# Performance work log

Hardware: AMD Instinct MI355X
Metric: run time of the kernel (lower is better)

Reference implementation:

```python
import jax, jax.numpy as jnp
import numpy as np

B, S, D, H = 4, 2048, 1024, 16
HD = D // H

def setup_inputs() -> dict:
    key = jax.random.key(0)
    ks = jax.random.split(key, 11)
    s = 1.0 / np.sqrt(D)
    return {
        "q": jax.random.normal(ks[0], (B, S, D), jnp.float32),
        "k": jax.random.normal(ks[1], (B, S, D), jnp.float32),
        "v": jax.random.normal(ks[2], (B, S, D), jnp.float32),
        "Wq": jax.random.normal(ks[3], (D, D), jnp.float32) * s,
        "bq": jax.random.normal(ks[4], (D,), jnp.float32) * 0.01,
        "Wk": jax.random.normal(ks[5], (D, D), jnp.float32) * s,
        "bk": jax.random.normal(ks[6], (D,), jnp.float32) * 0.01,
        "Wv": jax.random.normal(ks[7], (D, D), jnp.float32) * s,
        "bv": jax.random.normal(ks[8], (D,), jnp.float32) * 0.01,
        "Wo": jax.random.normal(ks[9], (D, D), jnp.float32) * s,
        "bo": jax.random.normal(ks[10], (D,), jnp.float32) * 0.01,
    }

def reference(q, k, v, Wq, bq, Wk, bk, Wv, bv, Wo, bo):
    # linear projections + ReLU activation (as in the torch module)
    qh = jax.nn.relu(q @ Wq.T + bq)
    kh = jax.nn.relu(k @ Wk.T + bk)
    vh = jax.nn.relu(v @ Wv.T + bv)
    # split heads: [B,S,D] -> [B,H,S,HD]
    def split(x):
        return x.reshape(B, S, H, HD).transpose(0, 2, 1, 3)
    qh, kh, vh = split(qh), split(kh), split(vh)
    scale = 1.0 / np.sqrt(HD).astype(np.float32)
    scores = jnp.einsum("bhqd,bhkd->bhqk", qh, kh) * scale
    attn = jax.nn.softmax(scores, axis=-1)
    y = jnp.einsum("bhqk,bhkd->bhqd", attn, vh)
    # merge heads: [B,H,S,HD] -> [B,S,D]
    y = y.transpose(0, 2, 1, 3).reshape(B, S, D)
    return jax.nn.relu(y @ Wo.T + bo)
```

## Files before the change

### kernel.cpp

```cpp
#include <hip/hip_runtime.h>
#include <hip/hip_bf16.h>
#include <cstdint>
#include <cstddef>

#define Bc 4
#define Sc 2048
#define Dc 1024
#define Hc 16

typedef __bf16 bf16;
typedef bf16  bf16x4 __attribute__((ext_vector_type(4)));
typedef bf16  bf16x8 __attribute__((ext_vector_type(8)));
typedef float f32x4  __attribute__((ext_vector_type(4)));

__device__ __forceinline__ void load_lds16(const bf16* g, bf16* l) {
    __builtin_amdgcn_global_load_lds((const __attribute__((address_space(1))) void*)g,
                                     (__attribute__((address_space(3))) void*)l,
                                     16, 0, 0);
}

__device__ __forceinline__ void cvt16(const float* __restrict__ g,
                                      bf16x8& lo, bf16x8& hi) {
    const f32x4 a0 = *(const f32x4*)(g);
    const f32x4 a1 = *(const f32x4*)(g + 4);
    const f32x4 a2 = *(const f32x4*)(g + 8);
    const f32x4 a3 = *(const f32x4*)(g + 12);
#pragma unroll
    for (int j = 0; j < 4; j++) {
        lo[j]     = (bf16)a0[j];
        lo[j + 4] = (bf16)a1[j];
        hi[j]     = (bf16)a2[j];
        hi[j + 4] = (bf16)a3[j];
    }
}

__device__ __forceinline__ void store_relu(float* p, float v) { *p = fmaxf(v, 0.0f); }
__device__ __forceinline__ void store_relu(bf16*  p, float v) { *p = (bf16)fmaxf(v, 0.0f); }

__global__ __launch_bounds__(256)
void cvt_f32_bf16(const float* __restrict__ src, bf16* __restrict__ dst, int n16) {
    const int idx = blockIdx.x * 256 + threadIdx.x;
    if (idx >= n16) return;
    bf16x8 lo, hi;
    cvt16(src + (size_t)idx * 16, lo, hi);
    *(bf16x8*)(dst + (size_t)idx * 16)     = lo;
    *(bf16x8*)(dst + (size_t)idx * 16 + 8) = hi;
}

#define BM 128
#define BN 128
#define BK 64

template <typename TC, bool TR>
__global__ __launch_bounds__(256)
void gemm_bb(const bf16* __restrict__ A, const bf16* __restrict__ W,
             const float* __restrict__ bias, TC* __restrict__ C,
             int M, int N, int K) {
    constexpr int POOL = TR ? 36864 : 32768;
    __shared__ __align__(16) char pool[POOL];
    bf16* lA = (bf16*)pool;
    bf16* lB = (bf16*)(pool + 16384);

    const int t    = threadIdx.x;
    const int lane = t & 63;
    const int wave = t >> 6;
    const int l15  = lane & 15;
    const int quad = lane >> 4;

    const int m0 = blockIdx.x * BM;
    const int n0 = blockIdx.y * BN;
    const int wm = (wave >> 1) * 64;
    const int wn = (wave & 1) * 64;

    f32x4 acc[4][4] = {};

    const int srow = t >> 3;
    const int cg   = (((t & 7) ^ (srow & 7)) << 3);
    const bf16* gA = A + (size_t)(m0 + srow) * K + cg;
    const bf16* gW = W + (size_t)(n0 + srow) * K + cg;
    bf16* lA0 = lA + t * 8;
    bf16* lB0 = lB + t * 8;

    for (int k0 = 0; k0 < K; k0 += BK) {
        __syncthreads();
#pragma unroll
        for (int c = 0; c < 4; c++) {
            load_lds16(gA + (size_t)(32 * c) * K, lA0 + c * 2048);
            load_lds16(gW + (size_t)(32 * c) * K, lB0 + c * 2048);
        }
        gA += BK; gW += BK;
        __syncthreads();

#pragma unroll
        for (int ks = 0; ks < 2; ks++) {
            bf16x8 af[4], bfr[4];
#pragma unroll
            for (int mt = 0; mt < 4; mt++) {
                const int row = wm + mt * 16 + l15;
                const int colp = ((((ks << 2) | quad) ^ (l15 & 7)) << 3);
                af[mt] = *(const bf16x8*)(lA + row * BK + colp);
            }
#pragma unroll
            for (int nt = 0; nt < 4; nt++) {
                const int row = wn + nt * 16 + l15;
                const int colp = ((((ks << 2) | quad) ^ (l15 & 7)) << 3);
                bfr[nt] = *(const bf16x8*)(lB + row * BK + colp);
            }
#pragma unroll
            for (int mt = 0; mt < 4; mt++)
#pragma unroll
                for (int nt = 0; nt < 4; nt++)
                    acc[mt][nt] = __builtin_amdgcn_mfma_f32_16x16x32_bf16(
                        af[mt], bfr[nt], acc[mt][nt], 0, 0, 0);
        }
    }

    if constexpr (!TR) {
#pragma unroll
        for (int nt = 0; nt < 4; nt++) {
            const int col = n0 + wn + nt * 16 + l15;
            const float bv = bias[col];
#pragma unroll
            for (int mt = 0; mt < 4; mt++) {
                const int rowb = m0 + wm + mt * 16 + quad * 4;
#pragma unroll
                for (int i = 0; i < 4; i++)
                    store_relu(&C[(size_t)(rowb + i) * N + col], acc[mt][nt][i] + bv);
            }
        }
    } else {
        __syncthreads();
        bf16* trp = (bf16*)pool;
#pragma unroll
        for (int nt = 0; nt < 4; nt++) {
            const int col = n0 + wn + nt * 16 + l15;
            const float bv = bias[col];
#pragma unroll
            for (int mt = 0; mt < 4; mt++)
#pragma unroll
                for (int i = 0; i < 4; i++)
                    trp[((wave * 64) + nt * 16 + l15) * 72 + mt * 16 + quad * 4 + i] =
                        (bf16)fmaxf(acc[mt][nt][i] + bv, 0.0f);
        }
        __syncthreads();
        const int r2 = lane >> 3;
        const int c8 = (lane & 7) * 8;
#pragma unroll
        for (int rr = 0; rr < 8; rr++) {
            const int rt = rr * 8 + r2;
            const bf16x8 vv = *(const bf16x8*)&trp[((wave * 64) + rt) * 72 + c8];
            const int cg2 = n0 + wn + rt;
            const int h   = cg2 >> 6, hd = cg2 & 63;
            const int mg  = m0 + wm + c8;
            const int b   = mg >> 11, s = mg & (Sc - 1);
            bf16* dst = (bf16*)C + ((size_t)(b * Hc + h) * 64 + hd) * Sc + s;
            *(bf16x8*)dst = vv;
        }
    }
}

__global__ __launch_bounds__(256)
void attn_flash(const bf16* __restrict__ Qh, const bf16* __restrict__ Kh,
                const bf16* __restrict__ Vt_g, bf16* __restrict__ Y) {
    __shared__ __align__(16) bf16 Kl[64][72];
    __shared__ __align__(16) bf16 Vl[64][72];
    __shared__ __align__(16) bf16 Pl[4][32][72];

    const int t    = threadIdx.x;
    const int lane = t & 63;
    const int wave = t >> 6;
    const int l15  = lane & 15;
    const int quad = lane >> 4;

    const int qt = blockIdx.x;
    const int bh = blockIdx.y;
    const int b  = bh >> 4;
    const int h  = bh & 15;
    const int q0 = qt * 128;
    const size_t rowbase = (size_t)b * Sc;
    const size_t vhead   = (size_t)(b * Hc + h) * 64;

    const float qscale = 0.125f * 1.44269504f;
    bf16x8 qf[2][2];
#pragma unroll
    for (int qi = 0; qi < 2; qi++) {
        const bf16* qp = Qh + (rowbase + q0 + wave * 32 + qi * 16 + l15) * (size_t)Dc + h * 64;
#pragma unroll
        for (int ks = 0; ks < 2; ks++) {
            const bf16x8 raw = *(const bf16x8*)(qp + ks * 32 + quad * 8);
#pragma unroll
            for (int j = 0; j < 8; j++) qf[qi][ks][j] = (bf16)((float)raw[j] * qscale);
        }
    }

    float lrun[2] = {0.0f, 0.0f};
    f32x4 yacc[2][4] = {};

    const int sr = t >> 2;
    const int sc = (t & 3) * 16;

    for (int kt = 0; kt < Sc / 64; kt++) {
        const int kb = kt * 64;
        const bf16* kp = Kh + (rowbase + kb + sr) * (size_t)Dc + h * 64 + sc;
        const bf16* vp = Vt_g + (vhead + sr) * (size_t)Sc + kb + sc;
        const bf16x8 k0 = *(const bf16x8*)kp;
        const bf16x8 k1 = *(const bf16x8*)(kp + 8);
        const bf16x8 v0 = *(const bf16x8*)vp;
        const bf16x8 v1 = *(const bf16x8*)(vp + 8);
        __syncthreads();
        *(bf16x8*)&Kl[sr][sc]     = k0;
        *(bf16x8*)&Kl[sr][sc + 8] = k1;
        *(bf16x8*)&Vl[sr][sc]     = v0;
        *(bf16x8*)&Vl[sr][sc + 8] = v1;
        __syncthreads();

        bf16x8 kf[4][2];
#pragma unroll
        for (int mt = 0; mt < 4; mt++) {
            kf[mt][0] = *(const bf16x8*)&Kl[mt * 16 + l15][quad * 8];
            kf[mt][1] = *(const bf16x8*)&Kl[mt * 16 + l15][32 + quad * 8];
        }

        f32x4 s[2][4];
#pragma unroll
        for (int qi = 0; qi < 2; qi++)
#pragma unroll
            for (int mt = 0; mt < 4; mt++) {
                s[qi][mt] = (f32x4){0.f, 0.f, 0.f, 0.f};
                s[qi][mt] = __builtin_amdgcn_mfma_f32_16x16x32_bf16(
                    kf[mt][0], qf[qi][0], s[qi][mt], 0, 0, 0);
                s[qi][mt] = __builtin_amdgcn_mfma_f32_16x16x32_bf16(
                    kf[mt][1], qf[qi][1], s[qi][mt], 0, 0, 0);
            }

#pragma unroll
        for (int qi = 0; qi < 2; qi++) {
            float sum = 0.f;
#pragma unroll
            for (int mt = 0; mt < 4; mt++) {
#pragma unroll
                for (int i = 0; i < 4; i++) {
                    const float p = exp2f(s[qi][mt][i]);
                    s[qi][mt][i] = p;
                    sum += p;
                }
                bf16x4 pk;
#pragma unroll
                for (int i = 0; i < 4; i++) pk[i] = (bf16)s[qi][mt][i];
                *(bf16x4*)&Pl[wave][qi * 16 + l15][mt * 16 + quad * 4] = pk;
            }
            lrun[qi] += sum;
        }

        bf16x8 vf[4][2];
#pragma unroll
        for (int nt = 0; nt < 4; nt++) {
            vf[nt][0] = *(const bf16x8*)&Vl[nt * 16 + l15][quad * 8];
            vf[nt][1] = *(const bf16x8*)&Vl[nt * 16 + l15][32 + quad * 8];
        }

#pragma unroll
        for (int qi = 0; qi < 2; qi++)
#pragma unroll
            for (int ks = 0; ks < 2; ks++) {
                const bf16x8 pf = *(const bf16x8*)&Pl[wave][qi * 16 + l15][ks * 32 + quad * 8];
#pragma unroll
                for (int nt = 0; nt < 4; nt++)
                    yacc[qi][nt] = __builtin_amdgcn_mfma_f32_16x16x32_bf16(
                        vf[nt][ks], pf, yacc[qi][nt], 0, 0, 0);
            }
    }

#pragma unroll
    for (int qi = 0; qi < 2; qi++) {
        float l = lrun[qi];
        l += __shfl_xor(l, 16);
        l += __shfl_xor(l, 32);
        const float inv = 1.0f / l;
        bf16* yp = Y + (rowbase + q0 + wave * 32 + qi * 16 + l15) * (size_t)Dc + h * 64;
#pragma unroll
        for (int nt = 0; nt < 4; nt++)
#pragma unroll
            for (int i = 0; i < 4; i++)
                yp[nt * 16 + quad * 4 + i] = (bf16)(yacc[qi][nt][i] * inv);
    }
}

extern "C" void kernel_launch(void* const* d_in, const int* in_sizes, int n_in,
                              void* d_out, int out_size, void* d_ws, size_t ws_size,
                              hipStream_t stream) {
    const float* q  = (const float*)d_in[0];
    const float* k  = (const float*)d_in[1];
    const float* v  = (const float*)d_in[2];
    const float* Wq = (const float*)d_in[3];
    const float* bq = (const float*)d_in[4];
    const float* Wk = (const float*)d_in[5];
    const float* bk = (const float*)d_in[6];
    const float* Wv = (const float*)d_in[7];
    const float* bv = (const float*)d_in[8];
    const float* Wo = (const float*)d_in[9];
    const float* bo = (const float*)d_in[10];
    float* out = (float*)d_out;

    const int M = Bc * Sc;
    const int N = Dc;
    const int K = Dc;
    const size_t E  = (size_t)Bc * Sc * Dc;
    const size_t EW = (size_t)Dc * Dc;

    bf16* Qh   = (bf16*)d_out;
    bf16* Kh   = Qh + E;
    bf16* tmpA = (bf16*)d_ws;
    bf16* VtG  = tmpA + E;
    bf16* Wqb  = VtG + E;
    bf16* Wkb  = Wqb + EW;
    bf16* Wvb  = Wkb + EW;
    bf16* Wob  = Wvb + EW;

    const int n16  = (int)(E / 16);
    const int n16w = (int)(EW / 16);
    dim3 gc(n16 / 256);
    dim3 gw(n16w / 256);
    dim3 gg(M / BM, N / BN);
    dim3 ga(Sc / 128, Bc * Hc);

    cvt_f32_bf16<<<gw, 256, 0, stream>>>(Wq, Wqb, n16w);
    cvt_f32_bf16<<<gw, 256, 0, stream>>>(Wk, Wkb, n16w);
    cvt_f32_bf16<<<gw, 256, 0, stream>>>(Wv, Wvb, n16w);
    cvt_f32_bf16<<<gw, 256, 0, stream>>>(Wo, Wob, n16w);

    cvt_f32_bf16<<<gc, 256, 0, stream>>>(q, tmpA, n16);
    gemm_bb<bf16, false><<<gg, 256, 0, stream>>>(tmpA, Wqb, bq, Qh, M, N, K);

    cvt_f32_bf16<<<gc, 256, 0, stream>>>(k, tmpA, n16);
    gemm_bb<bf16, false><<<gg, 256, 0, stream>>>(tmpA, Wkb, bk, Kh, M, N, K);

    cvt_f32_bf16<<<gc, 256, 0, stream>>>(v, tmpA, n16);
    gemm_bb<bf16, true><<<gg, 256, 0, stream>>>(tmpA, Wvb, bv, VtG, M, N, K);

    attn_flash<<<ga, 256, 0, stream>>>(Qh, Kh, VtG, tmpA);

    gemm_bb<float, false><<<gg, 256, 0, stream>>>(tmpA, Wob, bo, out, M, N, K);
}
```

Baseline: 389.7 us.

## Fuse input conversion into batched QKV GEMM and split-K attention across waves

Merges the four weight conversions into one launch and folds the fp32-to-bf16 activation conversion into a single QKV GEMM launch with a z-dimension selecting Q, K or V. The A operand is now loaded as fp32 through registers and converted on the fly instead of being staged through a separate conversion pass. The attention kernel is restructured so each block handles 64 queries while its four waves split the key range and load tiles asynchronously into per-wave LDS, with partial results reduced through LDS at the end. This removes three full-tensor conversion passes and several launches. The costs are less latency hiding on A loads in the GEMM and a serial LDS reduction in attention.

```diff
diff --git a/kernel.cpp b/kernel.cpp
--- a/kernel.cpp
+++ b/kernel.cpp
@@ -38,26 +38,32 @@
 __device__ __forceinline__ void store_relu(bf16*  p, float v) { *p = (bf16)fmaxf(v, 0.0f); }
 
 __global__ __launch_bounds__(256)
-void cvt_f32_bf16(const float* __restrict__ src, bf16* __restrict__ dst, int n16) {
+void cvt_w4(const float* __restrict__ w0, const float* __restrict__ w1,
+            const float* __restrict__ w2, const float* __restrict__ w3,
+            bf16* __restrict__ dst, int n16) {
+    const int wi = blockIdx.y;
+    const float* src = (wi == 0) ? w0 : (wi == 1) ? w1 : (wi == 2) ? w2 : w3;
+    bf16* d = dst + (size_t)wi * Dc * Dc;
     const int idx = blockIdx.x * 256 + threadIdx.x;
     if (idx >= n16) return;
     bf16x8 lo, hi;
     cvt16(src + (size_t)idx * 16, lo, hi);
-    *(bf16x8*)(dst + (size_t)idx * 16)     = lo;
-    *(bf16x8*)(dst + (size_t)idx * 16 + 8) = hi;
+    *(bf16x8*)(d + (size_t)idx * 16)     = lo;
+    *(bf16x8*)(d + (size_t)idx * 16 + 8) = hi;
 }
 
 #define BM 128
 #define BN 128
 #define BK 64
 
-template <typename TC, bool TR>
 __global__ __launch_bounds__(256)
-void gemm_bb(const bf16* __restrict__ A, const bf16* __restrict__ W,
-             const float* __restrict__ bias, TC* __restrict__ C,
-             int M, int N, int K) {
-    constexpr int POOL = TR ? 36864 : 32768;
-    __shared__ __align__(16) char pool[POOL];
+void qkv_gemm(const float* __restrict__ Aq, const float* __restrict__ Ak,
+              const float* __restrict__ Av, const bf16* __restrict__ Wcat,
+              const float* __restrict__ b0, const float* __restrict__ b1,
+              const float* __restrict__ b2,
+              bf16* __restrict__ Qh, bf16* __restrict__ Kh, bf16* __restrict__ VtG,
+              int M, int N, int K) {
+    __shared__ __align__(16) char pool[36864];
     bf16* lA = (bf16*)pool;
     bf16* lB = (bf16*)(pool + 16384);
 
@@ -66,6 +72,11 @@
     const int wave = t >> 6;
     const int l15  = lane & 15;
     const int quad = lane >> 4;
+    const int z    = blockIdx.z;
+
+    const float* A    = (z == 0) ? Aq : (z == 1) ? Ak : Av;
+    const bf16*  W    = Wcat + (size_t)z * Dc * Dc;
+    const float* bias = (z == 0) ? b0 : (z == 1) ? b1 : b2;
 
     const int m0 = blockIdx.x * BM;
     const int n0 = blockIdx.y * BN;
@@ -74,38 +85,49 @@
 
     f32x4 acc[4][4] = {};
 
+    const int fr = t >> 1;
+    const int fh = (t & 1);
+    const float* gA = A + (size_t)(m0 + fr) * K + fh * 32;
+
     const int srow = t >> 3;
     const int cg   = (((t & 7) ^ (srow & 7)) << 3);
-    const bf16* gA = A + (size_t)(m0 + srow) * K + cg;
     const bf16* gW = W + (size_t)(n0 + srow) * K + cg;
-    bf16* lA0 = lA + t * 8;
     bf16* lB0 = lB + t * 8;
 
     for (int k0 = 0; k0 < K; k0 += BK) {
-        __syncthreads();
-#pragma unroll
-        for (int c = 0; c < 4; c++) {
-            load_lds16(gA + (size_t)(32 * c) * K, lA0 + c * 2048);
+        f32x4 a[8];
+#pragma unroll
+        for (int g = 0; g < 8; g++) a[g] = *(const f32x4*)(gA + g * 4);
+        gA += BK;
+        __syncthreads();
+#pragma unroll
+        for (int c = 0; c < 4; c++)
             load_lds16(gW + (size_t)(32 * c) * K, lB0 + c * 2048);
-        }
-        gA += BK; gW += BK;
+        gW += BK;
+#pragma unroll
+        for (int j = 0; j < 4; j++) {
+            bf16x8 pk;
+#pragma unroll
+            for (int e = 0; e < 4; e++) {
+                pk[e]     = (bf16)a[2 * j][e];
+                pk[e + 4] = (bf16)a[2 * j + 1][e];
+            }
+            const int G = fh * 4 + j;
+            const int p = G ^ (fr & 7);
+            *(bf16x8*)(lA + fr * BK + p * 8) = pk;
+        }
         __syncthreads();
 
 #pragma unroll
         for (int ks = 0; ks < 2; ks++) {
+            const int colp = ((((ks << 2) | quad) ^ (l15 & 7)) << 3);
             bf16x8 af[4], bfr[4];
 #pragma unroll
-            for (int mt = 0; mt < 4; mt++) {
-                const int row = wm + mt * 16 + l15;
-                const int colp = ((((ks << 2) | quad) ^ (l15 & 7)) << 3);
-                af[mt] = *(const bf16x8*)(lA + row * BK + colp);
-            }
-#pragma unroll
-            for (int nt = 0; nt < 4; nt++) {
-                const int row = wn + nt * 16 + l15;
-                const int colp = ((((ks << 2) | quad) ^ (l15 & 7)) << 3);
-                bfr[nt] = *(const bf16x8*)(lB + row * BK + colp);
-            }
+            for (int mt = 0; mt < 4; mt++)
+                af[mt] = *(const bf16x8*)(lA + (wm + mt * 16 + l15) * BK + colp);
+#pragma unroll
+            for (int nt = 0; nt < 4; nt++)
+                bfr[nt] = *(const bf16x8*)(lB + (wn + nt * 16 + l15) * BK + colp);
 #pragma unroll
             for (int mt = 0; mt < 4; mt++)
 #pragma unroll
@@ -115,7 +137,8 @@
         }
     }
 
-    if constexpr (!TR) {
+    if (z < 2) {
+        bf16* C = (z == 0) ? Qh : Kh;
 #pragma unroll
         for (int nt = 0; nt < 4; nt++) {
             const int col = n0 + wn + nt * 16 + l15;
@@ -125,7 +148,7 @@
                 const int rowb = m0 + wm + mt * 16 + quad * 4;
 #pragma unroll
                 for (int i = 0; i < 4; i++)
-                    store_relu(&C[(size_t)(rowb + i) * N + col], acc[mt][nt][i] + bv);
+                    C[(size_t)(rowb + i) * N + col] = (bf16)fmaxf(acc[mt][nt][i] + bv, 0.0f);
             }
         }
     } else {
@@ -153,18 +176,19 @@
             const int h   = cg2 >> 6, hd = cg2 & 63;
             const int mg  = m0 + wm + c8;
             const int b   = mg >> 11, s = mg & (Sc - 1);
-            bf16* dst = (bf16*)C + ((size_t)(b * Hc + h) * 64 + hd) * Sc + s;
+            bf16* dst = VtG + ((size_t)(b * Hc + h) * 64 + hd) * Sc + s;
             *(bf16x8*)dst = vv;
         }
     }
 }
 
 __global__ __launch_bounds__(256)
-void attn_flash(const bf16* __restrict__ Qh, const bf16* __restrict__ Kh,
-                const bf16* __restrict__ Vt_g, bf16* __restrict__ Y) {
-    __shared__ __align__(16) bf16 Kl[64][72];
-    __shared__ __align__(16) bf16 Vl[64][72];
-    __shared__ __align__(16) bf16 Pl[4][32][72];
+void gemm_out(const bf16* __restrict__ A, const bf16* __restrict__ W,
+              const float* __restrict__ bias, float* __restrict__ C,
+              int M, int N, int K) {
+    __shared__ __align__(16) char pool[32768];
+    bf16* lA = (bf16*)pool;
+    bf16* lB = (bf16*)(pool + 16384);
 
     const int t    = threadIdx.x;
     const int lane = t & 63;
@@ -172,117 +196,232 @@
     const int l15  = lane & 15;
     const int quad = lane >> 4;
 
+    const int m0 = blockIdx.x * BM;
+    const int n0 = blockIdx.y * BN;
+    const int wm = (wave >> 1) * 64;
+    const int wn = (wave & 1) * 64;
+
+    f32x4 acc[4][4] = {};
+
+    const int srow = t >> 3;
+    const int cg   = (((t & 7) ^ (srow & 7)) << 3);
+    const bf16* gA = A + (size_t)(m0 + srow) * K + cg;
+    const bf16* gW = W + (size_t)(n0 + srow) * K + cg;
+    bf16* lA0 = lA + t * 8;
+    bf16* lB0 = lB + t * 8;
+
+    for (int k0 = 0; k0 < K; k0 += BK) {
+        __syncthreads();
+#pragma unroll
+        for (int c = 0; c < 4; c++) {
+            load_lds16(gA + (size_t)(32 * c) * K, lA0 + c * 2048);
+            load_lds16(gW + (size_t)(32 * c) * K, lB0 + c * 2048);
+        }
+        gA += BK; gW += BK;
+        __syncthreads();
+
+#pragma unroll
+        for (int ks = 0; ks < 2; ks++) {
+            const int colp = ((((ks << 2) | quad) ^ (l15 & 7)) << 3);
+            bf16x8 af[4], bfr[4];
+#pragma unroll
+            for (int mt = 0; mt < 4; mt++)
+                af[mt] = *(const bf16x8*)(lA + (wm + mt * 16 + l15) * BK + colp);
+#pragma unroll
+            for (int nt = 0; nt < 4; nt++)
+                bfr[nt] = *(const bf16x8*)(lB + (wn + nt * 16 + l15) * BK + colp);
+#pragma unroll
+            for (int mt = 0; mt < 4; mt++)
+#pragma unroll
+                for (int nt = 0; nt < 4; nt++)
+                    acc[mt][nt] = __builtin_amdgcn_mfma_f32_16x16x32_bf16(
+                        af[mt], bfr[nt], acc[mt][nt], 0, 0, 0);
+        }
+    }
+
+#pragma unroll
+    for (int nt = 0; nt < 4; nt++) {
+        const int col = n0 + wn + nt * 16 + l15;
+        const float bv = bias[col];
+#pragma unroll
+        for (int mt = 0; mt < 4; mt++) {
+            const int rowb = m0 + wm + mt * 16 + quad * 4;
+#pragma unroll
+            for (int i = 0; i < 4; i++)
+                store_relu(&C[(size_t)(rowb + i) * N + col], acc[mt][nt][i] + bv);
+        }
+    }
+}
+
+__global__ __launch_bounds__(256)
+void attn_flash(const bf16* __restrict__ Qh, const bf16* __restrict__ Kh,
+                const bf16* __restrict__ Vt_g, bf16* __restrict__ Y) {
+    __shared__ __align__(16) bf16 pool[4 * 2048 + 4 * 2048 + 4 * 2304];
+    bf16* Kw = pool;
+    bf16* Vw = pool + 8192;
+    bf16* Pw = pool + 16384;
+
+    const int t    = threadIdx.x;
+    const int lane = t & 63;
+    const int wave = t >> 6;
+    const int l15  = lane & 15;
+    const int quad = lane >> 4;
+
     const int qt = blockIdx.x;
     const int bh = blockIdx.y;
     const int b  = bh >> 4;
     const int h  = bh & 15;
-    const int q0 = qt * 128;
+    const int q0 = qt * 64;
     const size_t rowbase = (size_t)b * Sc;
     const size_t vhead   = (size_t)(b * Hc + h) * 64;
 
     const float qscale = 0.125f * 1.44269504f;
-    bf16x8 qf[2][2];
-#pragma unroll
-    for (int qi = 0; qi < 2; qi++) {
-        const bf16* qp = Qh + (rowbase + q0 + wave * 32 + qi * 16 + l15) * (size_t)Dc + h * 64;
+    bf16x8 qf[4][2];
+#pragma unroll
+    for (int qi = 0; qi < 4; qi++) {
+        const bf16* qp = Qh + (rowbase + q0 + qi * 16 + l15) * (size_t)Dc + h * 64;
 #pragma unroll
         for (int ks = 0; ks < 2; ks++) {
             const bf16x8 raw = *(const bf16x8*)(qp + ks * 32 + quad * 8);
-#pragma unroll
-            for (int j = 0; j < 8; j++) qf[qi][ks][j] = (bf16)((float)raw[j] * qscale);
-        }
-    }
-
-    float lrun[2] = {0.0f, 0.0f};
-    f32x4 yacc[2][4] = {};
-
-    const int sr = t >> 2;
-    const int sc = (t & 3) * 16;
-
-    for (int kt = 0; kt < Sc / 64; kt++) {
-        const int kb = kt * 64;
-        const bf16* kp = Kh + (rowbase + kb + sr) * (size_t)Dc + h * 64 + sc;
-        const bf16* vp = Vt_g + (vhead + sr) * (size_t)Sc + kb + sc;
-        const bf16x8 k0 = *(const bf16x8*)kp;
-        const bf16x8 k1 = *(const bf16x8*)(kp + 8);
-        const bf16x8 v0 = *(const bf16x8*)vp;
-        const bf16x8 v1 = *(const bf16x8*)(vp + 8);
-        __syncthreads();
-        *(bf16x8*)&Kl[sr][sc]     = k0;
-        *(bf16x8*)&Kl[sr][sc + 8] = k1;
-        *(bf16x8*)&Vl[sr][sc]     = v0;
-        *(bf16x8*)&Vl[sr][sc + 8] = v1;
-        __syncthreads();
-
-        bf16x8 kf[4][2];
-#pragma unroll
-        for (int mt = 0; mt < 4; mt++) {
-            kf[mt][0] = *(const bf16x8*)&Kl[mt * 16 + l15][quad * 8];
-            kf[mt][1] = *(const bf16x8*)&Kl[mt * 16 + l15][32 + quad * 8];
-        }
-
-        f32x4 s[2][4];
-#pragma unroll
-        for (int qi = 0; qi < 2; qi++)
-#pragma unroll
-            for (int mt = 0; mt < 4; mt++) {
-                s[qi][mt] = (f32x4){0.f, 0.f, 0.f, 0.f};
-                s[qi][mt] = __builtin_amdgcn_mfma_f32_16x16x32_bf16(
-                    kf[mt][0], qf[qi][0], s[qi][mt], 0, 0, 0);
-                s[qi][mt] = __builtin_amdgcn_mfma_f32_16x16x32_bf16(
-                    kf[mt][1], qf[qi][1], s[qi][mt], 0, 0, 0);
-            }
-
-#pragma unroll
-        for (int qi = 0; qi < 2; qi++) {
+            bf16x8 sc;
+#pragma unroll
+            for (int j = 0; j < 8; j++) sc[j] = (bf16)((float)raw[j] * qscale);
+            qf[qi][ks] = sc;
+        }
+    }
+
+    float lrun[4] = {0.f, 0.f, 0.f, 0.f};
+    f32x4 yacc[4][4] = {};
+
+    bf16* KwW = Kw + wave * 2048;
+    bf16* VwW = Vw + wave * 2048;
+    bf16* PwW = Pw + wave * 2304;
+
+    const int kR = lane >> 3;
+    const int kG = (lane & 7) ^ (kR & 7);
+    const int vR = lane >> 2;
+    const int vG = (lane & 3) ^ ((lane >> 3) & 3);
+
+    for (int kt = wave; kt < Sc / 32; kt += 4) {
+        const int kb = kt * 32;
+#pragma unroll
+        for (int c = 0; c < 4; c++) {
+            const int r = 8 * c + kR;
+            load_lds16(Kh + (rowbase + kb + r) * (size_t)Dc + h * 64 + kG * 8,
+                       KwW + c * 512 + lane * 8);
+        }
+#pragma unroll
+        for (int c = 0; c < 4; c++) {
+            const int r = 16 * c + vR;
+            load_lds16(Vt_g + (vhead + r) * (size_t)Sc + kb + vG * 8,
+                       VwW + c * 512 + lane * 8);
+        }
+        asm volatile("s_waitcnt vmcnt(0)" ::: "memory");
+
+        bf16x8 kf[2][2];
+#pragma unroll
+        for (int mt = 0; mt < 2; mt++)
+#pragma unroll
+            for (int ks = 0; ks < 2; ks++) {
+                const int p = ((ks << 2) | quad) ^ (l15 & 7);
+                kf[mt][ks] = *(const bf16x8*)(KwW + (mt * 16 + l15) * 64 + p * 8);
+            }
+        bf16x8 vf[4];
+#pragma unroll
+        for (int nt = 0; nt < 4; nt++) {
+            const int p = quad ^ ((l15 >> 1) & 3);
+            vf[nt] = *(const bf16x8*)(VwW + (nt * 16 + l15) * 32 + p * 8);
+        }
+
+#pragma unroll
+        for (int qi = 0; qi < 4; qi++) {
+            f32x4 s[2];
+#pragma unroll
+            for (int mt = 0; mt < 2; mt++) {
+                s[mt] = (f32x4){0.f, 0.f, 0.f, 0.f};
+                s[mt] = __builtin_amdgcn_mfma_f32_16x16x32_bf16(
+                    kf[mt][0], qf[qi][0], s[mt], 0, 0, 0);
+                s[mt] = __builtin_amdgcn_mfma_f32_16x16x32_bf16(
+                    kf[mt][1], qf[qi][1], s[mt], 0, 0, 0);
+            }
             float sum = 0.f;
 #pragma unroll
-            for (int mt = 0; mt < 4; mt++) {
+            for (int mt = 0; mt < 2; mt++) {
+                bf16x4 pk;
 #pragma unroll
                 for (int i = 0; i < 4; i++) {
-                    const float p = exp2f(s[qi][mt][i]);
-                    s[qi][mt][i] = p;
+                    const float p = exp2f(s[mt][i]);
                     sum += p;
+                    pk[i] = (bf16)p;
                 }
-                bf16x4 pk;
-#pragma unroll
-                for (int i = 0; i < 4; i++) pk[i] = (bf16)s[qi][mt][i];
-                *(bf16x4*)&Pl[wave][qi * 16 + l15][mt * 16 + quad * 4] = pk;
+                *(bf16x4*)(PwW + (qi * 16 + l15) * 36 + mt * 16 + quad * 4) = pk;
             }
             lrun[qi] += sum;
-        }
-
-        bf16x8 vf[4][2];
-#pragma unroll
-        for (int nt = 0; nt < 4; nt++) {
-            vf[nt][0] = *(const bf16x8*)&Vl[nt * 16 + l15][quad * 8];
-            vf[nt][1] = *(const bf16x8*)&Vl[nt * 16 + l15][32 + quad * 8];
-        }
-
-#pragma unroll
-        for (int qi = 0; qi < 2; qi++)
-#pragma unroll
-            for (int ks = 0; ks < 2; ks++) {
-                const bf16x8 pf = *(const bf16x8*)&Pl[wave][qi * 16 + l15][ks * 32 + quad * 8];
-#pragma unroll
-                for (int nt = 0; nt < 4; nt++)
-                    yacc[qi][nt] = __builtin_amdgcn_mfma_f32_16x16x32_bf16(
-                        vf[nt][ks], pf, yacc[qi][nt], 0, 0, 0);
-            }
-    }
-
-#pragma unroll
-    for (int qi = 0; qi < 2; qi++) {
-        float l = lrun[qi];
-        l += __shfl_xor(l, 16);
-        l += __shfl_xor(l, 32);
-        const float inv = 1.0f / l;
-        bf16* yp = Y + (rowbase + q0 + wave * 32 + qi * 16 + l15) * (size_t)Dc + h * 64;
-#pragma unroll
-        for (int nt = 0; nt < 4; nt++)
-#pragma unroll
-            for (int i = 0; i < 4; i++)
-                yp[nt * 16 + quad * 4 + i] = (bf16)(yacc[qi][nt][i] * inv);
+            const bf16x8 pf = *(const bf16x8*)(PwW + (qi * 16 + l15) * 36 + quad * 8);
+#pragma unroll
+            for (int nt = 0; nt < 4; nt++)
+                yacc[qi][nt] = __builtin_amdgcn_mfma_f32_16x16x32_bf16(
+                    vf[nt], pf, yacc[qi][nt], 0, 0, 0);
+        }
+    }
+
+    float* red = (float*)pool;
+    __syncthreads();
+    if (wave >= 2) {
+        float* my = red + (size_t)((wave - 2) * 64 + lane) * 68;
+#pragma unroll
+        for (int qi = 0; qi < 4; qi++)
+#pragma unroll
+            for (int nt = 0; nt < 4; nt++)
+                *(f32x4*)(my + (qi * 4 + nt) * 4) = yacc[qi][nt];
+        *(f32x4*)(my + 64) = (f32x4){lrun[0], lrun[1], lrun[2], lrun[3]};
+    }
+    __syncthreads();
+    if (wave < 2) {
+        const float* src = red + (size_t)(wave * 64 + lane) * 68;
+#pragma unroll
+        for (int qi = 0; qi < 4; qi++)
+#pragma unroll
+            for (int nt = 0; nt < 4; nt++)
+                yacc[qi][nt] += *(const f32x4*)(src + (qi * 4 + nt) * 4);
+        const f32x4 lr = *(const f32x4*)(src + 64);
+#pragma unroll
+        for (int qi = 0; qi < 4; qi++) lrun[qi] += lr[qi];
+    }
+    __syncthreads();
+    if (wave == 1) {
+        float* my = red + (size_t)lane * 68;
+#pragma unroll
+        for (int qi = 0; qi < 4; qi++)
+#pragma unroll
+            for (int nt = 0; nt < 4; nt++)
+                *(f32x4*)(my + (qi * 4 + nt) * 4) = yacc[qi][nt];
+        *(f32x4*)(my + 64) = (f32x4){lrun[0], lrun[1], lrun[2], lrun[3]};
+    }
+    __syncthreads();
+    if (wave == 0) {
+        const float* src = red + (size_t)lane * 68;
+#pragma unroll
+        for (int qi = 0; qi < 4; qi++)
+#pragma unroll
+            for (int nt = 0; nt < 4; nt++)
+                yacc[qi][nt] += *(const f32x4*)(src + (qi * 4 + nt) * 4);
+        const f32x4 lr = *(const f32x4*)(src + 64);
+#pragma unroll
+        for (int qi = 0; qi < 4; qi++) {
+            float l = lrun[qi] + lr[qi];
+            l += __shfl_xor(l, 16);
+            l += __shfl_xor(l, 32);
+            const float inv = 1.0f / l;
+            bf16* yp = Y + (rowbase + q0 + qi * 16 + l15) * (size_t)Dc + h * 64;
+#pragma unroll
+            for (int nt = 0; nt < 4; nt++) {
+                bf16x4 o;
+#pragma unroll
+                for (int i = 0; i < 4; i++) o[i] = (bf16)(yacc[qi][nt][i] * inv);
+                *(bf16x4*)(yp + nt * 16 + quad * 4) = o;
+            }
+        }
     }
 }
 
@@ -310,35 +449,19 @@
 
     bf16* Qh   = (bf16*)d_out;
     bf16* Kh   = Qh + E;
-    bf16* tmpA = (bf16*)d_ws;
-    bf16* VtG  = tmpA + E;
-    bf16* Wqb  = VtG + E;
-    bf16* Wkb  = Wqb + EW;
-    bf16* Wvb  = Wkb + EW;
-    bf16* Wob  = Wvb + EW;
-
-    const int n16  = (int)(E / 16);
+    bf16* Wcat = (bf16*)d_ws;
+    bf16* VtG  = Wcat + 4 * EW;
+    bf16* Yw   = VtG + E;
+
     const int n16w = (int)(EW / 16);
-    dim3 gc(n16 / 256);
-    dim3 gw(n16w / 256);
+    dim3 gw(n16w / 256, 4);
+    dim3 gqkv(M / BM, N / BN, 3);
+    dim3 ga(Sc / 64, Bc * Hc);
     dim3 gg(M / BM, N / BN);
-    dim3 ga(Sc / 128, Bc * Hc);
-
-    cvt_f32_bf16<<<gw, 256, 0, stream>>>(Wq, Wqb, n16w);
-    cvt_f32_bf16<<<gw, 256, 0, stream>>>(Wk, Wkb, n16w);
-    cvt_f32_bf16<<<gw, 256, 0, stream>>>(Wv, Wvb, n16w);
-    cvt_f32_bf16<<<gw, 256, 0, stream>>>(Wo, Wob, n16w);
-
-    cvt_f32_bf16<<<gc, 256, 0, stream>>>(q, tmpA, n16);
-    gemm_bb<bf16, false><<<gg, 256, 0, stream>>>(tmpA, Wqb, bq, Qh, M, N, K);
-
-    cvt_f32_bf16<<<gc, 256, 0, stream>>>(k, tmpA, n16);
-    gemm_bb<bf16, false><<<gg, 256, 0, stream>>>(tmpA, Wkb, bk, Kh, M, N, K);
-
-    cvt_f32_bf16<<<gc, 256, 0, stream>>>(v, tmpA, n16);
-    gemm_bb<bf16, true><<<gg, 256, 0, stream>>>(tmpA, Wvb, bv, VtG, M, N, K);
-
-    attn_flash<<<ga, 256, 0, stream>>>(Qh, Kh, VtG, tmpA);
-
-    gemm_bb<float, false><<<gg, 256, 0, stream>>>(tmpA, Wob, bo, out, M, N, K);
-}
+
+    cvt_w4<<<gw, 256, 0, stream>>>(Wq, Wk, Wv, Wo, Wcat, n16w);
+    qkv_gemm<<<gqkv, 256, 0, stream>>>(q, k, v, Wcat, bq, bk, bv,
+                                       Qh, Kh, VtG, M, N, K);
+    attn_flash<<<ga, 256, 0, stream>>>(Qh, Kh, VtG, Yw);
+    gemm_out<<<gg, 256, 0, stream>>>(Yw, Wcat + 3 * EW, bo, out, M, N, K);
+}
```

Measured after the change: 502.9 us. 29.1% more time.
